# Optimization experiments

Hardware: AMD Instinct MI355X
Metric: run time of the kernel (lower is better)

## Reference

```python
import jax, jax.numpy as jnp
import numpy as np

B, S, D, V, T, NS, NG = 16, 512, 400, 32000, 8, 30, 3


def setup_inputs() -> dict:
    key = jax.random.key(0)
    ks = jax.random.split(key, 14)
    w = 1.0 / np.sqrt(D)
    return {
        "encoded_hidden": jax.random.normal(ks[0], (1, B, D), jnp.float32) * 0.1,
        "encoded_outputs": jax.random.normal(ks[1], (B, S, D), jnp.float32) * 0.1,
        "story": jax.random.randint(ks[2], (B, S), 0, V),
        "trg_batches": jax.random.randint(ks[3], (B, NS, T), 0, V),
        "shared_emb": jax.random.normal(ks[4], (V, D), jnp.float32) * 0.1,
        "slot_emb": jax.random.normal(ks[5], (1, D), jnp.float32) * 0.1,
        "w_ih": jax.random.normal(ks[6], (3 * D, D), jnp.float32) * w,
        "w_hh": jax.random.normal(ks[7], (3 * D, D), jnp.float32) * w,
        "b_ih": jax.random.normal(ks[8], (3 * D,), jnp.float32) * w,
        "b_hh": jax.random.normal(ks[9], (3 * D,), jnp.float32) * w,
        "w_ratio_w": jax.random.normal(ks[10], (1, 3 * D), jnp.float32) * w,
        "w_ratio_b": jax.random.normal(ks[11], (1,), jnp.float32) * w,
        "w_gate_w": jax.random.normal(ks[12], (NG, D), jnp.float32) * w,
        "w_gate_b": jax.random.normal(ks[13], (NG,), jnp.float32) * w,
        "batch_size": B,
        "max_resp_len": T,
    }


def reference(encoded_hidden, encoded_outputs, story, trg_batches, shared_emb,
              slot_emb, w_ih, w_hh, b_ih, b_hh, w_ratio_w, w_ratio_b,
              w_gate_w, w_gate_b, batch_size, max_resp_len):
    # Original torch code returns inside the slot loop -> only slot 0 is decoded.
    # h0 is re-used as GRU initial state at EVERY step (no carried hidden), and
    # teacher forcing makes each step's input known, so all T steps vectorize.
    h0 = encoded_hidden[0]                         # (B, D)
    Bq, Tq = batch_size, max_resp_len
    Vq = shared_emb.shape[0]

    # decoder inputs: step 0 = slot embedding, steps 1..T-1 = emb(trg[:,0,i-1])
    x0 = jnp.broadcast_to(slot_emb, h0.shape)      # (B, D)
    xt = shared_emb[trg_batches[:, 0, : Tq - 1]]   # (B, T-1, D)
    X = jnp.concatenate([x0[:, None, :], xt], axis=1)  # (B, T, D)

    # GRU cell (torch gate order r, z, n), h0 broadcast over steps
    gi = X @ w_ih.T + b_ih                         # (B, T, 3D)
    gh = h0 @ w_hh.T + b_hh                        # (B, 3D)
    i_r, i_z, i_n = jnp.split(gi, 3, axis=-1)
    h_r, h_z, h_n = jnp.split(gh, 3, axis=-1)
    r = jax.nn.sigmoid(i_r + h_r[:, None, :])
    z = jax.nn.sigmoid(i_z + h_z[:, None, :])
    n = jnp.tanh(i_n + r * h_n[:, None, :])
    h = (1.0 - z) * n + z * h0[:, None, :]         # (B, T, D) decoder_state == hidden

    # attention over history (no length masking: all lens == S)
    scores = jnp.einsum('btd,bsd->bts', h, encoded_outputs)   # (B, T, S)
    probs = jax.nn.softmax(scores, axis=-1)
    # FAITHFUL to original bug: context uses raw scores, not probs
    context = jnp.einsum('bts,bsd->btd', scores, encoded_outputs)

    gate0 = context[:, 0, :] @ w_gate_w.T + w_gate_b          # (B, NG), step i==0

    p_vocab = jax.nn.softmax(h @ shared_emb.T, axis=-1)       # (B, T, V)
    p_gen = jax.nn.sigmoid(
        jnp.concatenate([h, context, X], axis=-1) @ w_ratio_w.T + w_ratio_b
    )                                                         # (B, T, 1)

    # pointer distribution: scatter_add probs onto vocab ids of the story
    p_ctx = jnp.zeros((Bq, Tq, Vq), p_vocab.dtype).at[
        jnp.arange(Bq)[:, None, None],
        jnp.arange(Tq)[None, :, None],
        story[:, None, :],
    ].add(probs)

    p_final = p_gen * p_vocab + (1.0 - p_gen) * p_ctx         # (B, T, V)

    ptr_outputs = jnp.zeros((NS, Bq, Tq, Vq), p_final.dtype).at[0].set(p_final)
    gate_outputs = jnp.zeros((NS, Bq, NG), gate0.dtype).at[0].set(gate0)
    return ptr_outputs, gate_outputs
```

## Files before the change

### kernel.cpp

```cpp
#include <hip/hip_runtime.h>

#define Bq 16
#define Sq 512
#define Dq 400
#define Vq 32000
#define Tq 8
#define NSq 30
#define NGq 3
#define BTq (Bq*Tq)
#define D3q (3*Dq)
#define SLICE 4096000
#define PTR_TOTAL (30ull*SLICE)
#define GATE_TOTAL (NSq*Bq*NGq)

#define NCOMPUTE 250
#define NZERO 1813
#define ZPER 16384

__device__ inline float sigmoidf_(float x) { return 1.0f / (1.0f + __expf(-x)); }

__device__ inline float blockReduceSum(float v, float* red) {
    int tid = threadIdx.x;
    #pragma unroll
    for (int o = 32; o > 0; o >>= 1) v += __shfl_down(v, o, 64);
    if ((tid & 63) == 0) red[tid >> 6] = v;
    __syncthreads();
    if (tid == 0) {
        float s = red[0];
        int nw = blockDim.x >> 6;
        for (int i = 1; i < nw; i++) s += red[i];
        red[0] = s;
    }
    __syncthreads();
    float r = red[0];
    __syncthreads();
    return r;
}

__device__ inline float blockReduceMax(float v, float* red) {
    int tid = threadIdx.x;
    #pragma unroll
    for (int o = 32; o > 0; o >>= 1) v = fmaxf(v, __shfl_down(v, o, 64));
    if ((tid & 63) == 0) red[tid >> 6] = v;
    __syncthreads();
    if (tid == 0) {
        float s = red[0];
        int nw = blockDim.x >> 6;
        for (int i = 1; i < nw; i++) s = fmaxf(s, red[i]);
        red[0] = s;
    }
    __syncthreads();
    float r = red[0];
    __syncthreads();
    return r;
}

__global__ void k_prep(const float* __restrict__ enc_hidden, const float* __restrict__ shared_emb,
                       const float* __restrict__ slot_emb, const float* __restrict__ w_ih,
                       const float* __restrict__ w_hh, const float* __restrict__ b_ih,
                       const float* __restrict__ b_hh, const int* __restrict__ trg,
                       float* __restrict__ h_out, float* __restrict__ hT_out,
                       float* __restrict__ X_out) {
    __shared__ float x_l[Dq], h0_l[Dq], gi_l[D3q], gh_l[D3q];
    int bt = blockIdx.x, b = bt >> 3, t = bt & 7;
    int tid = threadIdx.x;
    int tok = (t == 0) ? 0 : trg[b * NSq * Tq + (t - 1)];
    for (int d = tid; d < Dq; d += blockDim.x) {
        x_l[d] = (t == 0) ? slot_emb[d] : shared_emb[(size_t)tok * Dq + d];
        h0_l[d] = enc_hidden[b * Dq + d];
    }
    __syncthreads();
    for (int j = tid; j < D3q; j += blockDim.x) {
        const float4* wi4 = (const float4*)(w_ih + (size_t)j * Dq);
        const float4* wh4 = (const float4*)(w_hh + (size_t)j * Dq);
        float ai = b_ih[j], ah = b_hh[j];
        for (int q = 0; q < Dq / 4; ++q) {
            float4 pi = wi4[q], ph = wh4[q];
            int k = 4 * q;
            ai += x_l[k]*pi.x + x_l[k+1]*pi.y + x_l[k+2]*pi.z + x_l[k+3]*pi.w;
            ah += h0_l[k]*ph.x + h0_l[k+1]*ph.y + h0_l[k+2]*ph.z + h0_l[k+3]*ph.w;
        }
        gi_l[j] = ai; gh_l[j] = ah;
    }
    __syncthreads();
    for (int d = tid; d < Dq; d += blockDim.x) {
        float r = sigmoidf_(gi_l[d] + gh_l[d]);
        float z = sigmoidf_(gi_l[Dq + d] + gh_l[Dq + d]);
        float n = tanhf(gi_l[2 * Dq + d] + r * gh_l[2 * Dq + d]);
        float h = (1.0f - z) * n + z * h0_l[d];
        h_out[bt * Dq + d] = h;
        hT_out[d * BTq + bt] = h;
        X_out[bt * Dq + d] = x_l[d];
    }
}

__global__ void k_attn(const float* __restrict__ hbuf, const float* __restrict__ Xbuf,
                       const float* __restrict__ enc_out, const float* __restrict__ w_ratio_w,
                       const float* __restrict__ w_ratio_b, const float* __restrict__ w_gate_w,
                       const float* __restrict__ w_gate_b,
                       float* __restrict__ probs, float* __restrict__ pgen,
                       float* __restrict__ out_gate) {
    __shared__ float h_l[Dq], ctx_l[Dq], sc_l[Sq], red[8];
    int bt = blockIdx.x, b = bt >> 3, t = bt & 7;
    int tid = threadIdx.x;
    for (int d = tid; d < Dq; d += 512) h_l[d] = hbuf[bt * Dq + d];
    __syncthreads();
    {
        const float4* e4 = (const float4*)(enc_out + ((size_t)(b * Sq + tid)) * Dq);
        float acc = 0.0f;
        for (int q = 0; q < Dq / 4; ++q) {
            float4 p = e4[q];
            int k = 4 * q;
            acc += h_l[k]*p.x + h_l[k+1]*p.y + h_l[k+2]*p.z + h_l[k+3]*p.w;
        }
        sc_l[tid] = acc;
    }
    __syncthreads();
    float myv = sc_l[tid];
    float m = blockReduceMax(myv, red);
    float e = __expf(myv - m);
    float ssum = blockReduceSum(e, red);
    probs[bt * Sq + tid] = e / ssum;
    for (int d = tid; d < Dq; d += 512) {
        float acc = 0.0f;
        #pragma unroll 8
        for (int s = 0; s < Sq; ++s)
            acc += sc_l[s] * enc_out[((size_t)(b * Sq + s)) * Dq + d];
        ctx_l[d] = acc;
    }
    __syncthreads();
    {
        float part = 0.0f;
        for (int i = tid; i < D3q; i += 512) {
            float v = (i < Dq) ? h_l[i] : (i < 2 * Dq ? ctx_l[i - Dq] : Xbuf[bt * Dq + (i - 2 * Dq)]);
            part += v * w_ratio_w[i];
        }
        float tot = blockReduceSum(part, red);
        if (tid == 0) pgen[bt] = sigmoidf_(tot + w_ratio_b[0]);
    }
    if (t == 0) {
        for (int g = 0; g < NGq; ++g) {
            float part = 0.0f;
            for (int d = tid; d < Dq; d += 512) part += ctx_l[d] * w_gate_w[g * Dq + d];
            float tot = blockReduceSum(part, red);
            if (tid == 0) out_gate[b * NGq + g] = tot + w_gate_b[g];
        }
    }
}

__global__ void k_scatter(const int* __restrict__ story, const float* __restrict__ probs,
                          float* __restrict__ pctx) {
    int bt = blockIdx.x, b = bt >> 3, s = threadIdx.x;
    int tok = story[b * Sq + s];
    atomicAdd(&pctx[(size_t)bt * Vq + tok], probs[bt * Sq + s]);
}

#define TVL 128
#define CKL 40
__global__ __launch_bounds__(256) void k_logits(const float* __restrict__ hT,
                                                const float* __restrict__ emb,
                                                float* __restrict__ logits,
                                                float* __restrict__ out) {
    __shared__ float eT[CKL][132];
    __shared__ float hL[CKL][132];
    int bid = blockIdx.x;
    int tid = threadIdx.x;
    if (bid >= NCOMPUTE) {
        int zb = bid - NCOMPUTE;
        float4 z = make_float4(0.0f, 0.0f, 0.0f, 0.0f);
        if (zb < NZERO) {
            float4* dst = (float4*)(out + (size_t)SLICE);
            const size_t total = 29ull * SLICE / 4;
            size_t base = (size_t)zb * ZPER + tid;
            #pragma unroll
            for (int r = 0; r < ZPER / 256; ++r) {
                size_t idx = base + (size_t)r * 256;
                if (idx < total) dst[idx] = z;
            }
        } else {
            float4* g = (float4*)(out + PTR_TOTAL + Bq * NGq);
            for (int i = tid; i < (GATE_TOTAL - Bq * NGq) / 4; i += 256) g[i] = z;
        }
        return;
    }
    int v0 = bid * TVL;
    int tx = tid & 15, ty = tid >> 4;
    float acc[8][8];
    #pragma unroll
    for (int j = 0; j < 8; ++j)
        #pragma unroll
        for (int i = 0; i < 8; ++i) acc[j][i] = 0.0f;

    for (int c = 0; c < Dq / CKL; ++c) {
        int k0 = c * CKL;
        const float4* hg = (const float4*)(hT + (size_t)k0 * BTq);
        #pragma unroll
        for (int r = 0; r < 5; ++r) {
            int idx = tid + 256 * r;
            int k = idx >> 5, c4 = idx & 31;
            float4 vd = hg[idx];
            *(float4*)&hL[k][4 * c4] = vd;
        }
        #pragma unroll
        for (int r = 0; r < 5; ++r) {
            int idx = tid + 256 * r;
            int v = idx / 10, q = idx - 10 * v;
            float4 vd = *(const float4*)(emb + (size_t)(v0 + v) * Dq + k0 + 4 * q);
            eT[4*q+0][v] = vd.x; eT[4*q+1][v] = vd.y; eT[4*q+2][v] = vd.z; eT[4*q+3][v] = vd.w;
        }
        __syncthreads();
        #pragma unroll 4
        for (int k = 0; k < CKL; ++k) {
            float4 h0 = *(const float4*)&hL[k][8 * ty];
            float4 h1 = *(const float4*)&hL[k][8 * ty + 4];
            float4 e0 = *(const float4*)&eT[k][8 * tx];
            float4 e1 = *(const float4*)&eT[k][8 * tx + 4];
            float hv[8] = {h0.x, h0.y, h0.z, h0.w, h1.x, h1.y, h1.z, h1.w};
            float ev[8] = {e0.x, e0.y, e0.z, e0.w, e1.x, e1.y, e1.z, e1.w};
            #pragma unroll
            for (int j = 0; j < 8; ++j)
                #pragma unroll
                for (int i = 0; i < 8; ++i)
                    acc[j][i] += hv[j] * ev[i];
        }
        __syncthreads();
    }
    #pragma unroll
    for (int j = 0; j < 8; ++j) {
        int bt = 8 * ty + j;
        float* dst = logits + (size_t)bt * Vq + v0 + 8 * tx;
        *(float4*)dst       = make_float4(acc[j][0], acc[j][1], acc[j][2], acc[j][3]);
        *(float4*)(dst + 4) = make_float4(acc[j][4], acc[j][5], acc[j][6], acc[j][7]);
    }
}

__global__ void k_stats(const float* __restrict__ logits, float* __restrict__ rmax,
                        float* __restrict__ rinv) {
    __shared__ float red[8];
    int row = blockIdx.x, tid = threadIdx.x;
    const float* lr = logits + (size_t)row * Vq;
    float m = -1e30f;
    for (int v = tid; v < Vq; v += 256) m = fmaxf(m, lr[v]);
    m = blockReduceMax(m, red);
    float s = 0.0f;
    for (int v = tid; v < Vq; v += 256) s += __expf(lr[v] - m);
    s = blockReduceSum(s, red);
    if (tid == 0) { rmax[row] = m; rinv[row] = 1.0f / s; }
}

__global__ void k_combine(const float* __restrict__ logits, const float* __restrict__ pctx,
                          const float* __restrict__ rmax, const float* __restrict__ rinv,
                          const float* __restrict__ pgen, float* __restrict__ out) {
    int bt = blockIdx.y;
    int v = blockIdx.x * 256 + threadIdx.x;
    float m = rmax[bt], inv = rinv[bt], pg = pgen[bt];
    size_t idx = (size_t)bt * Vq + v;
    float pv = __expf(logits[idx] - m) * inv;
    out[idx] = pg * pv + (1.0f - pg) * pctx[idx];
}

extern "C" void kernel_launch(void* const* d_in, const int* in_sizes, int n_in,
                              void* d_out, int out_size, void* d_ws, size_t ws_size,
                              hipStream_t stream) {
    const float* enc_hidden = (const float*)d_in[0];
    const float* enc_out    = (const float*)d_in[1];
    const int*   story      = (const int*)d_in[2];
    const int*   trg        = (const int*)d_in[3];
    const float* shared_emb = (const float*)d_in[4];
    const float* slot_emb   = (const float*)d_in[5];
    const float* w_ih       = (const float*)d_in[6];
    const float* w_hh       = (const float*)d_in[7];
    const float* b_ih       = (const float*)d_in[8];
    const float* b_hh       = (const float*)d_in[9];
    const float* w_ratio_w  = (const float*)d_in[10];
    const float* w_ratio_b  = (const float*)d_in[11];
    const float* w_gate_w   = (const float*)d_in[12];
    const float* w_gate_b   = (const float*)d_in[13];

    float* out = (float*)d_out;

    float* ws = (float*)d_ws;
    float* logits_buf = ws;
    float* pctx_buf   = ws + (size_t)SLICE;
    float* h_buf      = ws + 2 * (size_t)SLICE;
    float* X_buf      = h_buf + 51200;
    float* probs_buf  = X_buf + 51200;
    float* pgen_buf   = probs_buf + 65536;
    float* rmax_buf   = pgen_buf + 128;
    float* rinv_buf   = rmax_buf + 128;
    float* hT_buf     = rinv_buf + 128;

    hipMemsetAsync(pctx_buf, 0, (size_t)SLICE * sizeof(float), stream);

    hipLaunchKernelGGL(k_prep, dim3(BTq), dim3(256), 0, stream,
                       enc_hidden, shared_emb, slot_emb, w_ih, w_hh, b_ih, b_hh, trg,
                       h_buf, hT_buf, X_buf);
    hipLaunchKernelGGL(k_attn, dim3(BTq), dim3(512), 0, stream,
                       h_buf, X_buf, enc_out, w_ratio_w, w_ratio_b, w_gate_w, w_gate_b,
                       probs_buf, pgen_buf, out + PTR_TOTAL);
    hipLaunchKernelGGL(k_scatter, dim3(BTq), dim3(Sq), 0, stream, story, probs_buf, pctx_buf);
    hipLaunchKernelGGL(k_logits, dim3(NCOMPUTE + NZERO + 1), dim3(256), 0, stream,
                       hT_buf, shared_emb, logits_buf, out);
    hipLaunchKernelGGL(k_stats, dim3(BTq), dim3(256), 0, stream, logits_buf, rmax_buf, rinv_buf);
    hipLaunchKernelGGL(k_combine, dim3(Vq / 256, BTq), dim3(256), 0, stream,
                       logits_buf, pctx_buf, rmax_buf, rinv_buf, pgen_buf, out);
}
```

Baseline: 804.1 us.

## Restructure GRU gate GEMV, fuse scatter into attention, merge softmax stats and combine

The GRU gate computation is split into a new kernel that reuses weight rows across the 8 timesteps of a batch, so w_ih is read once per batch instead of once per (b,t). The GRU nonlinearity now runs inside the attention kernel, and the pointer scatter-add is fused there too, which removes the probs/h/X buffers and the separate scatter launch. The softmax stats and final combine are merged into one per-row kernel with float4 I/O. This cuts launches and intermediate traffic, but the final kernel now uses only 128 blocks for a 16 MB pass, which may under-use the GPU's memory bandwidth.

```diff
diff --git a/kernel.cpp b/kernel.cpp
--- a/kernel.cpp
+++ b/kernel.cpp
@@ -8,7 +8,6 @@
 #define NSq 30
 #define NGq 3
 #define BTq (Bq*Tq)
-#define D3q (3*Dq)
 #define SLICE 4096000
 #define PTR_TOTAL (30ull*SLICE)
 #define GATE_TOTAL (NSq*Bq*NGq)
@@ -55,55 +54,78 @@
     return r;
 }
 
-__global__ void k_prep(const float* __restrict__ enc_hidden, const float* __restrict__ shared_emb,
-                       const float* __restrict__ slot_emb, const float* __restrict__ w_ih,
-                       const float* __restrict__ w_hh, const float* __restrict__ b_ih,
-                       const float* __restrict__ b_hh, const int* __restrict__ trg,
-                       float* __restrict__ h_out, float* __restrict__ hT_out,
-                       float* __restrict__ X_out) {
-    __shared__ float x_l[Dq], h0_l[Dq], gi_l[D3q], gh_l[D3q];
+__global__ __launch_bounds__(256) void k_gates(const float* __restrict__ enc_hidden,
+                                               const float* __restrict__ shared_emb,
+                                               const float* __restrict__ slot_emb,
+                                               const float* __restrict__ w_ih,
+                                               const float* __restrict__ w_hh,
+                                               const float* __restrict__ b_ih,
+                                               const float* __restrict__ b_hh,
+                                               const int* __restrict__ trg,
+                                               float* __restrict__ gi, float* __restrict__ gh) {
+    __shared__ float A[9][Dq];
+    __shared__ int toks[8];
+    int b = blockIdx.x >> 2, jt = blockIdx.x & 3;
+    int tid = threadIdx.x;
+    if (tid < 7) toks[tid + 1] = trg[b * (NSq * Tq) + tid];
+    __syncthreads();
+    for (int idx = tid; idx < 900; idx += 256) {
+        int r = idx / 100, q = idx - r * 100;
+        const float4* src;
+        if (r == 8)      src = (const float4*)(enc_hidden + b * Dq);
+        else if (r == 0) src = (const float4*)slot_emb;
+        else             src = (const float4*)(shared_emb + (size_t)toks[r] * Dq);
+        *(float4*)&A[r][4 * q] = src[q];
+    }
+    __syncthreads();
+    for (int o = tid; o < 2700; o += 256) {
+        int r = o / 300, jj = o - r * 300;
+        int j = jt * 300 + jj;
+        const float* w = (r == 8) ? w_hh : w_ih;
+        const float4* w4 = (const float4*)(w + (size_t)j * Dq);
+        const float4* a4 = (const float4*)&A[r][0];
+        float acc = (r == 8) ? b_hh[j] : b_ih[j];
+        #pragma unroll 4
+        for (int q = 0; q < Dq / 4; ++q) {
+            float4 wv = w4[q], av = a4[q];
+            acc += av.x * wv.x + av.y * wv.y + av.z * wv.z + av.w * wv.w;
+        }
+        if (r == 8) gh[b * 1200 + j] = acc;
+        else        gi[(b * 8 + r) * 1200 + j] = acc;
+    }
+}
+
+__global__ __launch_bounds__(512) void k_attn(const float* __restrict__ gi,
+                                              const float* __restrict__ gh,
+                                              const float* __restrict__ enc_hidden,
+                                              const float* __restrict__ shared_emb,
+                                              const float* __restrict__ slot_emb,
+                                              const int* __restrict__ trg,
+                                              const float* __restrict__ enc_out,
+                                              const int* __restrict__ story,
+                                              const float* __restrict__ w_ratio_w,
+                                              const float* __restrict__ w_ratio_b,
+                                              const float* __restrict__ w_gate_w,
+                                              const float* __restrict__ w_gate_b,
+                                              float* __restrict__ pctx, float* __restrict__ pgen,
+                                              float* __restrict__ hT, float* __restrict__ out_gate) {
+    __shared__ float h_l[Dq], ctx_l[Dq], x_l[Dq], sc_l[Sq], red[8];
     int bt = blockIdx.x, b = bt >> 3, t = bt & 7;
     int tid = threadIdx.x;
-    int tok = (t == 0) ? 0 : trg[b * NSq * Tq + (t - 1)];
-    for (int d = tid; d < Dq; d += blockDim.x) {
-        x_l[d] = (t == 0) ? slot_emb[d] : shared_emb[(size_t)tok * Dq + d];
-        h0_l[d] = enc_hidden[b * Dq + d];
-    }
-    __syncthreads();
-    for (int j = tid; j < D3q; j += blockDim.x) {
-        const float4* wi4 = (const float4*)(w_ih + (size_t)j * Dq);
-        const float4* wh4 = (const float4*)(w_hh + (size_t)j * Dq);
-        float ai = b_ih[j], ah = b_hh[j];
-        for (int q = 0; q < Dq / 4; ++q) {
-            float4 pi = wi4[q], ph = wh4[q];
-            int k = 4 * q;
-            ai += x_l[k]*pi.x + x_l[k+1]*pi.y + x_l[k+2]*pi.z + x_l[k+3]*pi.w;
-            ah += h0_l[k]*ph.x + h0_l[k+1]*ph.y + h0_l[k+2]*ph.z + h0_l[k+3]*ph.w;
-        }
-        gi_l[j] = ai; gh_l[j] = ah;
-    }
-    __syncthreads();
-    for (int d = tid; d < Dq; d += blockDim.x) {
-        float r = sigmoidf_(gi_l[d] + gh_l[d]);
-        float z = sigmoidf_(gi_l[Dq + d] + gh_l[Dq + d]);
-        float n = tanhf(gi_l[2 * Dq + d] + r * gh_l[2 * Dq + d]);
-        float h = (1.0f - z) * n + z * h0_l[d];
-        h_out[bt * Dq + d] = h;
-        hT_out[d * BTq + bt] = h;
-        X_out[bt * Dq + d] = x_l[d];
-    }
-}
-
-__global__ void k_attn(const float* __restrict__ hbuf, const float* __restrict__ Xbuf,
-                       const float* __restrict__ enc_out, const float* __restrict__ w_ratio_w,
-                       const float* __restrict__ w_ratio_b, const float* __restrict__ w_gate_w,
-                       const float* __restrict__ w_gate_b,
-                       float* __restrict__ probs, float* __restrict__ pgen,
-                       float* __restrict__ out_gate) {
-    __shared__ float h_l[Dq], ctx_l[Dq], sc_l[Sq], red[8];
-    int bt = blockIdx.x, b = bt >> 3, t = bt & 7;
-    int tid = threadIdx.x;
-    for (int d = tid; d < Dq; d += 512) h_l[d] = hbuf[bt * Dq + d];
+    if (tid < Dq) {
+        int d = tid;
+        float x = (t == 0) ? slot_emb[d]
+                           : shared_emb[(size_t)trg[b * (NSq * Tq) + (t - 1)] * Dq + d];
+        float h0 = enc_hidden[b * Dq + d];
+        const float* gib = gi + bt * 1200;
+        const float* ghb = gh + b * 1200;
+        float r_ = sigmoidf_(gib[d] + ghb[d]);
+        float z  = sigmoidf_(gib[Dq + d] + ghb[Dq + d]);
+        float n  = tanhf(gib[2 * Dq + d] + r_ * ghb[2 * Dq + d]);
+        float h  = (1.0f - z) * n + z * h0;
+        h_l[d] = h; x_l[d] = x;
+        hT[d * BTq + bt] = h;
+    }
     __syncthreads();
     {
         const float4* e4 = (const float4*)(enc_out + ((size_t)(b * Sq + tid)) * Dq);
@@ -120,7 +142,7 @@
     float m = blockReduceMax(myv, red);
     float e = __expf(myv - m);
     float ssum = blockReduceSum(e, red);
-    probs[bt * Sq + tid] = e / ssum;
+    atomicAdd(&pctx[(size_t)bt * Vq + story[b * Sq + tid]], e / ssum);
     for (int d = tid; d < Dq; d += 512) {
         float acc = 0.0f;
         #pragma unroll 8
@@ -131,8 +153,8 @@
     __syncthreads();
     {
         float part = 0.0f;
-        for (int i = tid; i < D3q; i += 512) {
-            float v = (i < Dq) ? h_l[i] : (i < 2 * Dq ? ctx_l[i - Dq] : Xbuf[bt * Dq + (i - 2 * Dq)]);
+        for (int i = tid; i < 1200; i += 512) {
+            float v = (i < Dq) ? h_l[i] : (i < 2 * Dq ? ctx_l[i - Dq] : x_l[i - 2 * Dq]);
             part += v * w_ratio_w[i];
         }
         float tot = blockReduceSum(part, red);
@@ -146,13 +168,6 @@
             if (tid == 0) out_gate[b * NGq + g] = tot + w_gate_b[g];
         }
     }
-}
-
-__global__ void k_scatter(const int* __restrict__ story, const float* __restrict__ probs,
-                          float* __restrict__ pctx) {
-    int bt = blockIdx.x, b = bt >> 3, s = threadIdx.x;
-    int tok = story[b * Sq + s];
-    atomicAdd(&pctx[(size_t)bt * Vq + tok], probs[bt * Sq + s]);
 }
 
 #define TVL 128
@@ -234,29 +249,30 @@
     }
 }
 
-__global__ void k_stats(const float* __restrict__ logits, float* __restrict__ rmax,
-                        float* __restrict__ rinv) {
+__global__ __launch_bounds__(512) void k_final(const float* __restrict__ logits,
+                                               const float* __restrict__ pctx,
+                                               const float* __restrict__ pgen,
+                                               float* __restrict__ out) {
     __shared__ float red[8];
-    int row = blockIdx.x, tid = threadIdx.x;
-    const float* lr = logits + (size_t)row * Vq;
+    int bt = blockIdx.x, tid = threadIdx.x;
+    const float* lr = logits + (size_t)bt * Vq;
     float m = -1e30f;
-    for (int v = tid; v < Vq; v += 256) m = fmaxf(m, lr[v]);
+    for (int v = tid; v < Vq; v += 512) m = fmaxf(m, lr[v]);
     m = blockReduceMax(m, red);
     float s = 0.0f;
-    for (int v = tid; v < Vq; v += 256) s += __expf(lr[v] - m);
+    for (int v = tid; v < Vq; v += 512) s += __expf(lr[v] - m);
     s = blockReduceSum(s, red);
-    if (tid == 0) { rmax[row] = m; rinv[row] = 1.0f / s; }
-}
-
-__global__ void k_combine(const float* __restrict__ logits, const float* __restrict__ pctx,
-                          const float* __restrict__ rmax, const float* __restrict__ rinv,
-                          const float* __restrict__ pgen, float* __restrict__ out) {
-    int bt = blockIdx.y;
-    int v = blockIdx.x * 256 + threadIdx.x;
-    float m = rmax[bt], inv = rinv[bt], pg = pgen[bt];
-    size_t idx = (size_t)bt * Vq + v;
-    float pv = __expf(logits[idx] - m) * inv;
-    out[idx] = pg * pv + (1.0f - pg) * pctx[idx];
+    float inv = 1.0f / s, pg = pgen[bt], cg = 1.0f - pg;
+    const float4* l4 = (const float4*)lr;
+    const float4* p4 = (const float4*)(pctx + (size_t)bt * Vq);
+    float4* o4 = (float4*)(out + (size_t)bt * Vq);
+    for (int i = tid; i < Vq / 4; i += 512) {
+        float4 lv = l4[i], pv = p4[i];
+        o4[i] = make_float4(pg * __expf(lv.x - m) * inv + cg * pv.x,
+                            pg * __expf(lv.y - m) * inv + cg * pv.y,
+                            pg * __expf(lv.z - m) * inv + cg * pv.z,
+                            pg * __expf(lv.w - m) * inv + cg * pv.w);
+    }
 }
 
 extern "C" void kernel_launch(void* const* d_in, const int* in_sizes, int n_in,
@@ -282,26 +298,22 @@
     float* ws = (float*)d_ws;
     float* logits_buf = ws;
     float* pctx_buf   = ws + (size_t)SLICE;
-    float* h_buf      = ws + 2 * (size_t)SLICE;
-    float* X_buf      = h_buf + 51200;
-    float* probs_buf  = X_buf + 51200;
-    float* pgen_buf   = probs_buf + 65536;
-    float* rmax_buf   = pgen_buf + 128;
-    float* rinv_buf   = rmax_buf + 128;
-    float* hT_buf     = rinv_buf + 128;
+    float* gi_buf     = ws + 2 * (size_t)SLICE;
+    float* gh_buf     = gi_buf + 153600;
+    float* hT_buf     = gh_buf + 19200;
+    float* pgen_buf   = hT_buf + 51200;
 
     hipMemsetAsync(pctx_buf, 0, (size_t)SLICE * sizeof(float), stream);
 
-    hipLaunchKernelGGL(k_prep, dim3(BTq), dim3(256), 0, stream,
+    hipLaunchKernelGGL(k_gates, dim3(64), dim3(256), 0, stream,
                        enc_hidden, shared_emb, slot_emb, w_ih, w_hh, b_ih, b_hh, trg,
-                       h_buf, hT_buf, X_buf);
+                       gi_buf, gh_buf);
     hipLaunchKernelGGL(k_attn, dim3(BTq), dim3(512), 0, stream,
-                       h_buf, X_buf, enc_out, w_ratio_w, w_ratio_b, w_gate_w, w_gate_b,
-                       probs_buf, pgen_buf, out + PTR_TOTAL);
-    hipLaunchKernelGGL(k_scatter, dim3(BTq), dim3(Sq), 0, stream, story, probs_buf, pctx_buf);
+                       gi_buf, gh_buf, enc_hidden, shared_emb, slot_emb, trg,
+                       enc_out, story, w_ratio_w, w_ratio_b, w_gate_w, w_gate_b,
+                       pctx_buf, pgen_buf, hT_buf, out + PTR_TOTAL);
     hipLaunchKernelGGL(k_logits, dim3(NCOMPUTE + NZERO + 1), dim3(256), 0, stream,
                        hT_buf, shared_emb, logits_buf, out);
-    hipLaunchKernelGGL(k_stats, dim3(BTq), dim3(256), 0, stream, logits_buf, rmax_buf, rinv_buf);
-    hipLaunchKernelGGL(k_combine, dim3(Vq / 256, BTq), dim3(256), 0, stream,
-                       logits_buf, pctx_buf, rmax_buf, rinv_buf, pgen_buf, out);
-}
+    hipLaunchKernelGGL(k_final, dim3(BTq), dim3(512), 0, stream,
+                       logits_buf, pctx_buf, pgen_buf, out);
+}
```

After: 766.7 us. 1.05x faster.
